# Kernel optimization log

Hardware: AMD Instinct MI355X
Metric: run time of the kernel (lower is better)

Reference implementation:

```python
import jax, jax.numpy as jnp
import numpy as np

B, N, E, H = 16, 1024, 1024, 16  # batch must equal num_heads due to the 'hbkd' einsum in the original
D = E // H


def setup_inputs() -> dict:
    key = jax.random.key(0)
    ks = jax.random.split(key, 9)
    s = 0.02
    return {
        "x": jax.random.normal(ks[0], (B, N, E), dtype=jnp.float32),
        "Wq": jax.random.normal(ks[1], (E, E), dtype=jnp.float32) * s,
        "bq": jax.random.normal(ks[2], (E,), dtype=jnp.float32) * s,
        "Wk": jax.random.normal(ks[3], (E, E), dtype=jnp.float32) * s,
        "bk": jax.random.normal(ks[4], (E,), dtype=jnp.float32) * s,
        "Wv": jax.random.normal(ks[5], (E, E), dtype=jnp.float32) * s,
        "bv": jax.random.normal(ks[6], (E,), dtype=jnp.float32) * s,
        "Wp": jax.random.normal(ks[7], (E, E), dtype=jnp.float32) * s,
        "bp": jax.random.normal(ks[8], (E,), dtype=jnp.float32) * s,
    }


def _split_heads(t):  # [b, n, (h d)] -> [b, h, n, d]
    b, n, e = t.shape
    return t.reshape(b, n, H, D).transpose(0, 2, 1, 3)


def reference(x, Wq, bq, Wk, bk, Wv, bv, Wp, bp):
    q = _split_heads(x @ Wq.T + bq)  # [b, h, n, d]
    k = _split_heads(x @ Wk.T + bk)
    v = _split_heads(x @ Wv.T + bv)
    # Faithful to original: K is contracted with its batch/head axes SWAPPED ('hbkd').
    energy = jnp.einsum('bhqd,hbkd->bhqk', q, k)  # [b, h, n, n]
    # Faithful: softmax over the HEAD axis (dim=1), scale applied AFTER softmax.
    scale = E ** 0.5
    att = jax.nn.softmax(energy, axis=1) / scale
    # dropout rate is 0.0 -> identity
    o = jnp.einsum('bhal,bhlv->bhav', att, v)  # [b, h, n, d]
    o = o.transpose(0, 2, 1, 3).reshape(B, N, E)  # [b, n, (h d)]
    return o @ Wp.T + bp
```

## Files before the change

### kernel.cpp

```cpp
#include <hip/hip_runtime.h>
#include <hip/hip_bf16.h>

#define DEVI __device__ __forceinline__

typedef float f32x4 __attribute__((ext_vector_type(4)));
typedef short bf16x8 __attribute__((ext_vector_type(8)));
typedef unsigned short u16x4 __attribute__((ext_vector_type(4)));


DEVI unsigned short f2bf(float f) {
  union { float f; unsigned u; } v; v.f = f;
  unsigned r = v.u + 0x7fffu + ((v.u >> 16) & 1u);
  return (unsigned short)(r >> 16);
}

DEVI float fexp2(float x) {
#if __has_builtin(__builtin_amdgcn_exp2f)
  return __builtin_amdgcn_exp2f(x);
#else
  return exp2f(x);
#endif
}

DEVI float frcp(float x) {
#if __has_builtin(__builtin_amdgcn_rcpf)
  return __builtin_amdgcn_rcpf(x);
#else
  return 1.0f / x;
#endif
}

DEVI unsigned cvtpk(float a, float b) {
  unsigned r;
  asm("v_cvt_pk_bf16_f32 %0, %1, %2" : "=v"(r) : "v"(a), "v"(b));
  return r;
}

DEVI void gload_lds16(const unsigned short* g, unsigned short* l) {
  __builtin_amdgcn_global_load_lds(
      (const __attribute__((address_space(1))) void*)g,
      (__attribute__((address_space(3))) void*)l, 16, 0, 0);
}

__global__ void cvt_kernel(const float* __restrict__ s, unsigned short* __restrict__ d, int n4) {
  int i = blockIdx.x * blockDim.x + threadIdx.x;
  const int st = gridDim.x * blockDim.x;
  for (; i < n4; i += st) {
    const float4 v = reinterpret_cast<const float4*>(s)[i];
    u16x4 o;
    o[0] = f2bf(v.x); o[1] = f2bf(v.y); o[2] = f2bf(v.z); o[3] = f2bf(v.w);
    reinterpret_cast<u16x4*>(d)[i] = o;
  }
}

DEVI void gemm_tile(const unsigned short* __restrict__ A,
                    const unsigned short* __restrict__ Bw,
                    int m0, int n0,
                    unsigned short* lsA, unsigned short* lsB,
                    f32x4 acc[4][4]) {
  const int tid = threadIdx.x;
  const int w = tid >> 6, l = tid & 63, lg = l >> 4, lr = l & 15;
  const int wr = w >> 1, wc = w & 1;
  for (int kt = 0; kt < 1024; kt += 64) {
#pragma unroll
    for (int i = 0; i < 4; i++) {
      const int c = i * 256 + tid;
      const int row = c >> 3, col = (c & 7) * 8;
      gload_lds16(&A[(m0 + row) * 1024 + kt + col], &lsA[(i * 256 + w * 64) * 8]);
      gload_lds16(&Bw[(n0 + row) * 1024 + kt + col], &lsB[(i * 256 + w * 64) * 8]);
    }
    __syncthreads();
#pragma unroll
    for (int ks = 0; ks < 2; ks++) {
      bf16x8 af[4], bf_[4];
#pragma unroll
      for (int fi = 0; fi < 4; fi++) af[fi] = *(const bf16x8*)&lsA[(wr * 64 + fi * 16 + lr) * 64 + ks * 32 + lg * 8];
#pragma unroll
      for (int fj = 0; fj < 4; fj++) bf_[fj] = *(const bf16x8*)&lsB[(wc * 64 + fj * 16 + lr) * 64 + ks * 32 + lg * 8];
#pragma unroll
      for (int fi = 0; fi < 4; fi++)
#pragma unroll
        for (int fj = 0; fj < 4; fj++)
          acc[fi][fj] = __builtin_amdgcn_mfma_f32_16x16x32_bf16(af[fi], bf_[fj], acc[fi][fj], 0, 0, 0);
    }
    __syncthreads();
  }
}

__global__ __launch_bounds__(256, 2) void proj_qkv(
    const unsigned short* __restrict__ X, const unsigned short* __restrict__ W3,
    const float* __restrict__ bq, const float* __restrict__ bk, const float* __restrict__ bv,
    unsigned short* __restrict__ outq, unsigned short* __restrict__ outk, unsigned short* __restrict__ outv) {
  __shared__ unsigned short lsA[128 * 64];
  __shared__ unsigned short lsB[128 * 64];
  const int z = blockIdx.z;
  const int m0 = blockIdx.x * 128, n0 = blockIdx.y * 128;
  const unsigned short* Bw = W3 + z * 1048576;
  f32x4 acc[4][4];
  const f32x4 z4 = {0.f, 0.f, 0.f, 0.f};
#pragma unroll
  for (int i = 0; i < 4; i++)
#pragma unroll
    for (int j = 0; j < 4; j++) acc[i][j] = z4;
  gemm_tile(X, Bw, m0, n0, lsA, lsB, acc);

  const int tid = threadIdx.x;
  const int w = tid >> 6, l = tid & 63, lg = l >> 4, lr = l & 15, wr = w >> 1, wc = w & 1;
  const float* bias = (z == 0) ? bq : ((z == 1) ? bk : bv);
  const float SC = 1.4426950408889634f;
#pragma unroll
  for (int fi = 0; fi < 4; fi++) {
    const int mb = m0 + wr * 64 + fi * 16 + lg * 4;
#pragma unroll
    for (int fj = 0; fj < 4; fj++) {
      const int ncol = n0 + wc * 64 + fj * 16 + lr;
      const float bsv = bias[ncol];
      const int h = ncol >> 6, d = ncol & 63;
      if (z == 0) {
        const int ks = d >> 5, lgq = (d >> 3) & 3, eq = d & 7;
#pragma unroll
        for (int r = 0; r < 4; r++) {
          const int m = mb + r;
          const int bb = m >> 10, nr = m & 1023;
          const int nt = nr >> 4, lrq = nr & 15;
          const int idx = (((bb * 64 + nt) * 32 + h * 2 + ks) * 64 + lgq * 16 + lrq) * 8 + eq;
          outq[idx] = f2bf((acc[fi][fj][r] + bsv) * SC);
        }
      } else if (z == 1) {
        const int ks = d >> 5, lhi = ((d >> 3) & 3) * 16, eq = d & 7;
#pragma unroll
        for (int r = 0; r < 4; r++) {
          const int m = mb + r;
          const int n = m & 1023, bx = m >> 10;
          const int lane = lhi + (n & 15);
          const int idx = ((((h * 64 + (n >> 4)) * 16 + bx) * 2 + ks) * 64 + lane) * 8 + eq;
          outk[idx] = f2bf(acc[fi][fj][r] + bsv);
        }
      } else {
        const int dt = d >> 4, lrv = d & 15;
        const int bb = mb >> 10, n = mb & 1023;
        const int kc = n >> 5, lgv = (n >> 3) & 3, ev = n & 7;
        u16x4 pk;
#pragma unroll
        for (int r = 0; r < 4; r++) pk[r] = f2bf(acc[fi][fj][r] + bsv);
        const int idx0 = ((((bb * 16 + h) * 32 + kc) * 4 + dt) * 64 + lgv * 16 + lrv) * 8 + ev;
        *(u16x4*)&outv[idx0] = pk;
      }
    }
  }
}

__global__ __launch_bounds__(256, 2) void proj_out(
    const unsigned short* __restrict__ A, const unsigned short* __restrict__ Wp,
    const float* __restrict__ bias, float* __restrict__ out) {
  __shared__ unsigned short lsA[128 * 64];
  __shared__ unsigned short lsB[128 * 64];
  const int m0 = blockIdx.x * 128, n0 = blockIdx.y * 128;
  f32x4 acc[4][4];
  const f32x4 z4 = {0.f, 0.f, 0.f, 0.f};
#pragma unroll
  for (int i = 0; i < 4; i++)
#pragma unroll
    for (int j = 0; j < 4; j++) acc[i][j] = z4;
  gemm_tile(A, Wp, m0, n0, lsA, lsB, acc);
  const int tid = threadIdx.x;
  const int w = tid >> 6, l = tid & 63, lg = l >> 4, lr = l & 15, wr = w >> 1, wc = w & 1;
#pragma unroll
  for (int fi = 0; fi < 4; fi++) {
    const int mb = m0 + wr * 64 + fi * 16 + lg * 4;
#pragma unroll
    for (int fj = 0; fj < 4; fj++) {
      const int ncol = n0 + wc * 64 + fj * 16 + lr;
      const float bsv = bias[ncol];
#pragma unroll
      for (int r = 0; r < 4; r++) out[(mb + r) * 1024 + ncol] = acc[fi][fj][r] + bsv;
    }
  }
}

__global__ __launch_bounds__(512, 2) void attn3(
    const unsigned short* __restrict__ Q2,
    const unsigned short* __restrict__ K2,
    const unsigned short* __restrict__ V2,
    unsigned short* __restrict__ O) {
  __shared__ unsigned short qlds[32768];
  __shared__ unsigned short abuf[32768];

  const int tid = threadIdx.x;
  const int w = tid >> 6, l = tid & 63;
  const int lr = l & 15, lg = l >> 4;
  const int bid = blockIdx.x;
  const int swz = (bid & 7) * 64 + (bid >> 3);
  const int b = swz >> 5, qt32 = swz & 31;
  const int qh = w >> 2, ksub = w & 3;

  {
    const unsigned short* qsrc = Q2 + (size_t)(b * 64 + qt32 * 2) * 16384 + (w * 64 + l) * 8;
    unsigned short* qdst = qlds + w * 512;
#pragma unroll
    for (int r = 0; r < 8; r++)
      gload_lds16(qsrc + r * 4096, qdst + r * 4096);
  }

  const int qwb = qh * 16 + lr;
  const int wswz = (qwb & 7) << 3;
  const int wbyte = qwb * 128 + (((ksub * 16 + lg * 4) ^ wswz) << 1);

  const f32x4 z4 = {0.f, 0.f, 0.f, 0.f};
  f32x4 oacc[2][2][4];
#pragma unroll
  for (int a = 0; a < 2; a++)
#pragma unroll
    for (int c = 0; c < 2; c++)
#pragma unroll
      for (int d = 0; d < 4; d++) oacc[a][c][d] = z4;

  __syncthreads();

  for (int it = 0; it < 16; it++) {
    int qo = 0;
    asm volatile("" : "+v"(qo));
    const int kt = it * 4 + ksub;
    const unsigned short* kp = K2 + (size_t)(b * 64 + kt) * 16384 + l * 8;

    f32x4 e[16];
#pragma unroll
    for (int h = 0; h < 16; h++) {
      bf16x8 q0 = *(const bf16x8*)((const char*)qlds + qo + (qh * 32 + h * 2 + 0) * 1024 + l * 16);
      bf16x8 q1 = *(const bf16x8*)((const char*)qlds + qo + (qh * 32 + h * 2 + 1) * 1024 + l * 16);
      bf16x8 k0 = *(const bf16x8*)(kp + (h * 2 + 0) * 512);
      bf16x8 k1 = *(const bf16x8*)(kp + (h * 2 + 1) * 512);
      f32x4 t = __builtin_amdgcn_mfma_f32_16x16x32_bf16(k0, q0, z4, 0, 0, 0);
      t = __builtin_amdgcn_mfma_f32_16x16x32_bf16(k1, q1, t, 0, 0, 0);
      t[0] = fexp2(t[0]); t[1] = fexp2(t[1]); t[2] = fexp2(t[2]); t[3] = fexp2(t[3]);
      e[h] = t;
    }
    f32x4 s = e[0];
#pragma unroll
    for (int h = 1; h < 16; h++) s += e[h];
    f32x4 inv;
    inv[0] = frcp(s[0]) * 0.03125f;
    inv[1] = frcp(s[1]) * 0.03125f;
    inv[2] = frcp(s[2]) * 0.03125f;
    inv[3] = frcp(s[3]) * 0.03125f;
    __syncthreads();
#pragma unroll
    for (int h = 0; h < 16; h++) {
      f32x4 v = e[h] * inv;
      uint2 pk;
      pk.x = cvtpk(v[0], v[1]);
      pk.y = cvtpk(v[2], v[3]);
      *(uint2*)((char*)abuf + h * 4096 + wbyte) = pk;
    }
    __syncthreads();
    const int kc0 = it * 2;
#pragma unroll
    for (int hh = 0; hh < 2; hh++) {
      const int h = w * 2 + hh;
      const char* vbp = (const char*)V2 + (size_t)(((b * 16 + h) * 32 + kc0) * 4) * 1024 + l * 16;
      bf16x8 vb[2][4];
#pragma unroll
      for (int kst = 0; kst < 2; kst++)
#pragma unroll
        for (int dt = 0; dt < 4; dt++)
          vb[kst][dt] = *(const bf16x8*)(vbp + (kst * 4 + dt) * 1024);
      bf16x8 pa[2][2];
#pragma unroll
      for (int qt = 0; qt < 2; qt++)
#pragma unroll
        for (int kst = 0; kst < 2; kst++)
          pa[qt][kst] = *(const bf16x8*)((const char*)abuf + h * 4096 + qt * 2048 + lr * 128 +
                                         (((kst * 4 + lg) ^ (lr & 7)) << 4));
#pragma unroll
      for (int qt = 0; qt < 2; qt++)
#pragma unroll
        for (int kst = 0; kst < 2; kst++)
#pragma unroll
          for (int dt = 0; dt < 4; dt++)
            oacc[hh][qt][dt] = __builtin_amdgcn_mfma_f32_16x16x32_bf16(pa[qt][kst], vb[kst][dt], oacc[hh][qt][dt], 0, 0, 0);
    }
  }

#pragma unroll
  for (int hh = 0; hh < 2; hh++) {
    const int h = w * 2 + hh;
#pragma unroll
    for (int qt = 0; qt < 2; qt++)
#pragma unroll
      for (int dt = 0; dt < 4; dt++)
#pragma unroll
        for (int r = 0; r < 4; r++) {
          const int n = qt32 * 32 + qt * 16 + lg * 4 + r;
          O[(size_t)(b * 1024 + n) * 1024 + h * 64 + dt * 16 + lr] = f2bf(oacc[hh][qt][dt][r]);
        }
  }
}

extern "C" void kernel_launch(void* const* d_in, const int* in_sizes, int n_in,
                              void* d_out, int out_size, void* d_ws, size_t ws_size,
                              hipStream_t stream) {
  const float* x  = (const float*)d_in[0];
  const float* Wq = (const float*)d_in[1];
  const float* bq = (const float*)d_in[2];
  const float* Wk = (const float*)d_in[3];
  const float* bk = (const float*)d_in[4];
  const float* Wv = (const float*)d_in[5];
  const float* bv = (const float*)d_in[6];
  const float* Wp = (const float*)d_in[7];
  const float* bp = (const float*)d_in[8];

  char* ws = (char*)d_ws;
  unsigned short* xbf  = (unsigned short*)(ws);
  unsigned short* qbf  = (unsigned short*)(ws + 33554432);
  unsigned short* kbf  = (unsigned short*)(ws + 67108864);
  unsigned short* vtbf = (unsigned short*)(ws + 100663296);
  unsigned short* wbf  = (unsigned short*)(ws + 134217728);

  cvt_kernel<<<2048, 256, 0, stream>>>(x, xbf, 4194304);
  cvt_kernel<<<512, 256, 0, stream>>>(Wq, wbf, 262144);
  cvt_kernel<<<512, 256, 0, stream>>>(Wk, wbf + 1048576, 262144);
  cvt_kernel<<<512, 256, 0, stream>>>(Wv, wbf + 2097152, 262144);
  cvt_kernel<<<512, 256, 0, stream>>>(Wp, wbf + 3145728, 262144);

  proj_qkv<<<dim3(128, 8, 3), 256, 0, stream>>>(xbf, wbf, bq, bk, bv, qbf, kbf, vtbf);
  attn3<<<512, 512, 0, stream>>>(qbf, kbf, vtbf, xbf);
  proj_out<<<dim3(128, 8, 1), 256, 0, stream>>>(xbf, wbf + 3145728, bp, (float*)d_out);
}
```

Before: 366.0 us.

## Split attention across 16 waves with cross-wave head-sum reduction in LDS

The attention kernel now runs 1024 threads per block instead of 512. Each wave owns four heads for both query halves instead of all sixteen heads for one half. The head-axis softmax denominator is therefore built as partial sums that are exchanged through LDS with an extra barrier, and each wave handles one head in the PV stage. The aim is to cut per-wave register pressure (fewer exp and accumulator registers) and raise parallelism, at the cost of more barriers and LDS traffic. The launch-bounds request of 4 blocks of 1024 threads may not be achievable, given the 128 KB of static LDS per block.

```diff
diff --git a/kernel.cpp b/kernel.cpp
--- a/kernel.cpp
+++ b/kernel.cpp
@@ -178,7 +178,7 @@
   }
 }
 
-__global__ __launch_bounds__(512, 2) void attn3(
+__global__ __launch_bounds__(1024, 4) void attn4(
     const unsigned short* __restrict__ Q2,
     const unsigned short* __restrict__ K2,
     const unsigned short* __restrict__ V2,
@@ -192,108 +192,115 @@
   const int bid = blockIdx.x;
   const int swz = (bid & 7) * 64 + (bid >> 3);
   const int b = swz >> 5, qt32 = swz & 31;
-  const int qh = w >> 2, ksub = w & 3;
+  const int ksub = w & 3, hq = w >> 2;
 
   {
-    const unsigned short* qsrc = Q2 + (size_t)(b * 64 + qt32 * 2) * 16384 + (w * 64 + l) * 8;
-    unsigned short* qdst = qlds + w * 512;
-#pragma unroll
-    for (int r = 0; r < 8; r++)
-      gload_lds16(qsrc + r * 4096, qdst + r * 4096);
-  }
-
-  const int qwb = qh * 16 + lr;
-  const int wswz = (qwb & 7) << 3;
-  const int wbyte = qwb * 128 + (((ksub * 16 + lg * 4) ^ wswz) << 1);
+    const unsigned short* qsrc = Q2 + (size_t)(b * 64 + qt32 * 2) * 16384 + tid * 8;
+    unsigned short* qdst = qlds + tid * 8;
+#pragma unroll
+    for (int r = 0; r < 4; r++) gload_lds16(qsrc + r * 8192, qdst + r * 8192);
+  }
+
+  const int kpart = ksub * 16 + lg * 4;
+  const int wswz = (lr & 7) << 3;
 
   const f32x4 z4 = {0.f, 0.f, 0.f, 0.f};
-  f32x4 oacc[2][2][4];
-#pragma unroll
-  for (int a = 0; a < 2; a++)
-#pragma unroll
-    for (int c = 0; c < 2; c++)
-#pragma unroll
-      for (int d = 0; d < 4; d++) oacc[a][c][d] = z4;
+  f32x4 oacc[2][4];
+#pragma unroll
+  for (int qt = 0; qt < 2; qt++)
+#pragma unroll
+    for (int dt = 0; dt < 4; dt++) oacc[qt][dt] = z4;
 
   __syncthreads();
 
+#pragma unroll 1
   for (int it = 0; it < 16; it++) {
     int qo = 0;
     asm volatile("" : "+v"(qo));
     const int kt = it * 4 + ksub;
     const unsigned short* kp = K2 + (size_t)(b * 64 + kt) * 16384 + l * 8;
 
-    f32x4 e[16];
-#pragma unroll
-    for (int h = 0; h < 16; h++) {
-      bf16x8 q0 = *(const bf16x8*)((const char*)qlds + qo + (qh * 32 + h * 2 + 0) * 1024 + l * 16);
-      bf16x8 q1 = *(const bf16x8*)((const char*)qlds + qo + (qh * 32 + h * 2 + 1) * 1024 + l * 16);
+    f32x4 e[4][2];
+#pragma unroll
+    for (int hl = 0; hl < 4; hl++) {
+      const int h = hq * 4 + hl;
       bf16x8 k0 = *(const bf16x8*)(kp + (h * 2 + 0) * 512);
       bf16x8 k1 = *(const bf16x8*)(kp + (h * 2 + 1) * 512);
-      f32x4 t = __builtin_amdgcn_mfma_f32_16x16x32_bf16(k0, q0, z4, 0, 0, 0);
-      t = __builtin_amdgcn_mfma_f32_16x16x32_bf16(k1, q1, t, 0, 0, 0);
-      t[0] = fexp2(t[0]); t[1] = fexp2(t[1]); t[2] = fexp2(t[2]); t[3] = fexp2(t[3]);
-      e[h] = t;
-    }
-    f32x4 s = e[0];
-#pragma unroll
-    for (int h = 1; h < 16; h++) s += e[h];
-    f32x4 inv;
-    inv[0] = frcp(s[0]) * 0.03125f;
-    inv[1] = frcp(s[1]) * 0.03125f;
-    inv[2] = frcp(s[2]) * 0.03125f;
-    inv[3] = frcp(s[3]) * 0.03125f;
-    __syncthreads();
-#pragma unroll
-    for (int h = 0; h < 16; h++) {
-      f32x4 v = e[h] * inv;
-      uint2 pk;
-      pk.x = cvtpk(v[0], v[1]);
-      pk.y = cvtpk(v[2], v[3]);
-      *(uint2*)((char*)abuf + h * 4096 + wbyte) = pk;
+#pragma unroll
+      for (int qh = 0; qh < 2; qh++) {
+        bf16x8 q0 = *(const bf16x8*)((const char*)qlds + qo + (qh * 32 + h * 2 + 0) * 1024 + l * 16);
+        bf16x8 q1 = *(const bf16x8*)((const char*)qlds + qo + (qh * 32 + h * 2 + 1) * 1024 + l * 16);
+        f32x4 t = __builtin_amdgcn_mfma_f32_16x16x32_bf16(k0, q0, z4, 0, 0, 0);
+        t = __builtin_amdgcn_mfma_f32_16x16x32_bf16(k1, q1, t, 0, 0, 0);
+        t[0] = fexp2(t[0]); t[1] = fexp2(t[1]); t[2] = fexp2(t[2]); t[3] = fexp2(t[3]);
+        e[hl][qh] = t;
+      }
+    }
+    f32x4 s0 = (e[0][0] + e[1][0]) + (e[2][0] + e[3][0]);
+    f32x4 s1 = (e[0][1] + e[1][1]) + (e[2][1] + e[3][1]);
+    __syncthreads();
+    *(f32x4*)((char*)abuf + (((ksub * 4 + hq) * 2 + 0) * 64 + l) * 16) = s0;
+    *(f32x4*)((char*)abuf + (((ksub * 4 + hq) * 2 + 1) * 64 + l) * 16) = s1;
+    __syncthreads();
+#pragma unroll
+    for (int p = 1; p < 4; p++) {
+      const int hqp = hq ^ p;
+      s0 += *(const f32x4*)((char*)abuf + (((ksub * 4 + hqp) * 2 + 0) * 64 + l) * 16);
+      s1 += *(const f32x4*)((char*)abuf + (((ksub * 4 + hqp) * 2 + 1) * 64 + l) * 16);
+    }
+    f32x4 inv0, inv1;
+    inv0[0] = frcp(s0[0]) * 0.03125f; inv0[1] = frcp(s0[1]) * 0.03125f;
+    inv0[2] = frcp(s0[2]) * 0.03125f; inv0[3] = frcp(s0[3]) * 0.03125f;
+    inv1[0] = frcp(s1[0]) * 0.03125f; inv1[1] = frcp(s1[1]) * 0.03125f;
+    inv1[2] = frcp(s1[2]) * 0.03125f; inv1[3] = frcp(s1[3]) * 0.03125f;
+    __syncthreads();
+#pragma unroll
+    for (int hl = 0; hl < 4; hl++) {
+      const int h = hq * 4 + hl;
+#pragma unroll
+      for (int qh = 0; qh < 2; qh++) {
+        f32x4 v = e[hl][qh] * (qh ? inv1 : inv0);
+        uint2 pk;
+        pk.x = cvtpk(v[0], v[1]);
+        pk.y = cvtpk(v[2], v[3]);
+        const int q = qh * 16 + lr;
+        *(uint2*)((char*)abuf + h * 4096 + q * 128 + ((kpart ^ wswz) << 1)) = pk;
+      }
     }
     __syncthreads();
     const int kc0 = it * 2;
-#pragma unroll
-    for (int hh = 0; hh < 2; hh++) {
-      const int h = w * 2 + hh;
-      const char* vbp = (const char*)V2 + (size_t)(((b * 16 + h) * 32 + kc0) * 4) * 1024 + l * 16;
-      bf16x8 vb[2][4];
+    const char* vbp = (const char*)V2 + (size_t)(((b * 16 + w) * 32 + kc0) * 4) * 1024 + l * 16;
+    bf16x8 vb[2][4];
+#pragma unroll
+    for (int kst = 0; kst < 2; kst++)
+#pragma unroll
+      for (int dt = 0; dt < 4; dt++)
+        vb[kst][dt] = *(const bf16x8*)(vbp + (kst * 4 + dt) * 1024);
+    bf16x8 pa[2][2];
+#pragma unroll
+    for (int qt = 0; qt < 2; qt++)
 #pragma unroll
       for (int kst = 0; kst < 2; kst++)
+        pa[qt][kst] = *(const bf16x8*)((const char*)abuf + w * 4096 + qt * 2048 + lr * 128 +
+                                       (((kst * 4 + lg) ^ (lr & 7)) << 4));
+#pragma unroll
+    for (int qt = 0; qt < 2; qt++)
+#pragma unroll
+      for (int kst = 0; kst < 2; kst++)
 #pragma unroll
         for (int dt = 0; dt < 4; dt++)
-          vb[kst][dt] = *(const bf16x8*)(vbp + (kst * 4 + dt) * 1024);
-      bf16x8 pa[2][2];
-#pragma unroll
-      for (int qt = 0; qt < 2; qt++)
-#pragma unroll
-        for (int kst = 0; kst < 2; kst++)
-          pa[qt][kst] = *(const bf16x8*)((const char*)abuf + h * 4096 + qt * 2048 + lr * 128 +
-                                         (((kst * 4 + lg) ^ (lr & 7)) << 4));
-#pragma unroll
-      for (int qt = 0; qt < 2; qt++)
-#pragma unroll
-        for (int kst = 0; kst < 2; kst++)
-#pragma unroll
-          for (int dt = 0; dt < 4; dt++)
-            oacc[hh][qt][dt] = __builtin_amdgcn_mfma_f32_16x16x32_bf16(pa[qt][kst], vb[kst][dt], oacc[hh][qt][dt], 0, 0, 0);
-    }
-  }
-
-#pragma unroll
-  for (int hh = 0; hh < 2; hh++) {
-    const int h = w * 2 + hh;
-#pragma unroll
-    for (int qt = 0; qt < 2; qt++)
-#pragma unroll
-      for (int dt = 0; dt < 4; dt++)
-#pragma unroll
-        for (int r = 0; r < 4; r++) {
-          const int n = qt32 * 32 + qt * 16 + lg * 4 + r;
-          O[(size_t)(b * 1024 + n) * 1024 + h * 64 + dt * 16 + lr] = f2bf(oacc[hh][qt][dt][r]);
-        }
-  }
+          oacc[qt][dt] = __builtin_amdgcn_mfma_f32_16x16x32_bf16(pa[qt][kst], vb[kst][dt], oacc[qt][dt], 0, 0, 0);
+  }
+
+#pragma unroll
+  for (int qt = 0; qt < 2; qt++)
+#pragma unroll
+    for (int dt = 0; dt < 4; dt++)
+#pragma unroll
+      for (int r = 0; r < 4; r++) {
+        const int n = qt32 * 32 + qt * 16 + lg * 4 + r;
+        O[(size_t)(b * 1024 + n) * 1024 + w * 64 + dt * 16 + lr] = f2bf(oacc[qt][dt][r]);
+      }
 }
 
 extern "C" void kernel_launch(void* const* d_in, const int* in_sizes, int n_in,
@@ -323,6 +330,6 @@
   cvt_kernel<<<512, 256, 0, stream>>>(Wp, wbf + 3145728, 262144);
 
   proj_qkv<<<dim3(128, 8, 3), 256, 0, stream>>>(xbf, wbf, bq, bk, bv, qbf, kbf, vtbf);
-  attn3<<<512, 512, 0, stream>>>(qbf, kbf, vtbf, xbf);
+  attn4<<<512, 1024, 0, stream>>>(qbf, kbf, vtbf, xbf);
   proj_out<<<dim3(128, 8, 1), 256, 0, stream>>>(xbf, wbf + 3145728, bp, (float*)d_out);
 }
```

After: 352.1 us. -3.8%, faster.
